# Kernel tuning notes

Hardware: AMD Instinct MI355X
Metric: run time of the kernel (lower is better)

## Reference

```python
import jax, jax.numpy as jnp
import numpy as np

N = 100000      # total nodes across batch of graphs
E = 1600000     # total edges (avg degree 16)
DIN = 16        # raw node feature dim
H = 128         # social_hidden_dim
HEADS = 4
DOUT = H // HEADS
LAYERS = 2
G = 64          # number of graphs in batch
FOUT = 256      # fusion_hidden_dim
NEG_SLOPE = 0.2


def layer_norm(x, g, b, eps=1e-5):
    mu = x.mean(-1, keepdims=True)
    var = ((x - mu) ** 2).mean(-1, keepdims=True)
    return (x - mu) / jnp.sqrt(var + eps) * g + b


def gat_conv(h, src, dst, W, a_src, a_dst, bias):
    # h: [N,H]; src/dst: [E+N] (self-loops included)
    hp = (h @ W).reshape(N, HEADS, DOUT)                    # [N,heads,dout]
    al_s = jnp.einsum('nhd,hd->nh', hp, a_src)              # [N,heads]
    al_d = jnp.einsum('nhd,hd->nh', hp, a_dst)
    logits = jax.nn.leaky_relu(al_s[src] + al_d[dst], NEG_SLOPE)  # [Etot,heads]
    m = jax.ops.segment_max(logits, dst, num_segments=N)    # segment softmax over dst
    e = jnp.exp(logits - m[dst])
    denom = jax.ops.segment_sum(e, dst, num_segments=N)
    alpha = e / (denom[dst] + 1e-16)                        # [Etot,heads]
    msg = hp[src] * alpha[:, :, None]                       # [Etot,heads,dout]
    out = jax.ops.segment_sum(msg, dst, num_segments=N)     # scatter-add
    return out.reshape(N, H) + bias


def setup_inputs():
    key = jax.random.key(0)
    ks = jax.random.split(key, 24)
    s = 0.05
    inp = {
        'x': jax.random.normal(ks[0], (N, DIN), jnp.float32),
        'edge_index': jax.random.randint(ks[1], (2, E), 0, N, jnp.int32),
        'node2graph': (jnp.arange(N, dtype=jnp.int32) * G // N).astype(jnp.int32),
        'Wp': jax.random.normal(ks[2], (DIN, H)) * s,
        'bp': jnp.zeros((H,)),
        'Wq1': jax.random.normal(ks[3], (2 * H, H)) * s,
        'bq1': jnp.zeros((H,)),
        'gq': jnp.ones((H,)), 'beq': jnp.zeros((H,)),
        'Wq2': jax.random.normal(ks[4], (H, FOUT)) * s,
        'bq2': jnp.zeros((FOUT,)),
    }
    for i in range(LAYERS):
        inp[f'Wg{i}'] = jax.random.normal(ks[5 + 4 * i], (H, H)) * s
        inp[f'as{i}'] = jax.random.normal(ks[6 + 4 * i], (HEADS, DOUT)) * s
        inp[f'ad{i}'] = jax.random.normal(ks[7 + 4 * i], (HEADS, DOUT)) * s
        inp[f'bg{i}'] = jnp.zeros((H,))
        inp[f'g{i}'] = jnp.ones((H,))
        inp[f'be{i}'] = jnp.zeros((H,))
    return inp


def reference(x, edge_index, node2graph, Wp, bp, Wq1, bq1, gq, beq, Wq2, bq2,
              Wg0, as0, ad0, bg0, g0, be0, Wg1, as1, ad1, bg1, g1, be1):
    loop = jnp.arange(N, dtype=edge_index.dtype)
    src = jnp.concatenate([edge_index[0], loop])  # add self-loops (PyG default)
    dst = jnp.concatenate([edge_index[1], loop])

    h = jax.nn.gelu(x @ Wp + bp, approximate=False)
    params = [(Wg0, as0, ad0, bg0, g0, be0), (Wg1, as1, ad1, bg1, g1, be1)]
    for (W, a_s, a_d, b, g, be) in params:
        h_new = gat_conv(h, src, dst, W, a_s, a_d, b)
        h = layer_norm(h_new + h, g, be)  # dims match -> residual

    counts = jax.ops.segment_sum(jnp.ones((N, 1), h.dtype), node2graph, num_segments=G)
    mean_pool = jax.ops.segment_sum(h, node2graph, num_segments=G) / jnp.maximum(counts, 1.0)
    max_pool = jax.ops.segment_max(h, node2graph, num_segments=G)
    emb = jnp.concatenate([mean_pool, max_pool], axis=-1)  # [G, 2H]

    p = layer_norm(emb @ Wq1 + bq1, gq, beq)
    p = jax.nn.gelu(p, approximate=False)
    return p @ Wq2 + bq2  # [G, FOUT]
```

## Files before the change

kernel.cpp:

```cpp
#include <hip/hip_runtime.h>

typedef unsigned short u16;
typedef unsigned char u8;
typedef unsigned int u32;
typedef unsigned long long u64;
typedef short short8 __attribute__((ext_vector_type(8)));
typedef float f32x4 __attribute__((ext_vector_type(4)));
typedef float f32x2 __attribute__((ext_vector_type(2)));

#define NN   100000
#define EE   1600000
#define ETOT (EE + NN)
#define NG   64
#define WSTR 136
#define SCANB 98
#define NB   98
#define BCAP 24576
#define OCAP 262144
#define EPB  4096

constexpr size_t AL256(size_t x) { return (x + 255) & ~(size_t)255; }
constexpr size_t OFF_FLAG   = 0;
constexpr size_t OFF_BSUM   = AL256(OFF_FLAG + 256);
constexpr size_t OFF_BCNT   = AL256(OFF_BSUM + 128 * 4);
constexpr size_t OFF_ROWPTR = AL256(OFF_BCNT + 128 * 4);
constexpr size_t OFF_DEG    = AL256(OFF_ROWPTR + (size_t)(NN + 1) * 4);
constexpr size_t OFF_COL    = AL256(OFF_DEG + (size_t)NN * 4);
constexpr size_t OFF_ALS    = AL256(OFF_COL + (size_t)ETOT * 4);
constexpr size_t OFF_ALD    = AL256(OFF_ALS + (size_t)NN * 4 * 4);
constexpr size_t OFF_GSUM   = AL256(OFF_ALD + (size_t)NN * 4 * 4);
constexpr size_t OFF_GKEY   = AL256(OFF_GSUM + (size_t)NG * 128 * 4);
constexpr size_t OFF_GCNT   = AL256(OFF_GKEY + (size_t)NG * 128 * 4);
constexpr size_t OFF_H      = AL256(OFF_GCNT + (size_t)NG * 4);
constexpr size_t OFF_HPB    = AL256(OFF_H + (size_t)NN * 128 * 2);
constexpr size_t OFF_EBUF   = AL256(OFF_HPB + (size_t)NN * 128 * 1);
constexpr size_t OFF_OBUF   = AL256(OFF_EBUF + (size_t)NB * BCAP * 8);
constexpr size_t WS_TOTAL   = AL256(OFF_OBUF + (size_t)OCAP * 8);

__device__ u64 g_ws[WS_TOTAL / 8];

__device__ __forceinline__ char* wsp() { return (char*)g_ws; }
#define WS_FLAG   ((int*)(wsp() + OFF_FLAG))
#define WS_BSUM   ((int*)(wsp() + OFF_BSUM))
#define WS_BCNT   ((int*)(wsp() + OFF_BCNT))
#define WS_ROWPTR ((int*)(wsp() + OFF_ROWPTR))
#define WS_DEG    ((int*)(wsp() + OFF_DEG))
#define WS_COL    ((int*)(wsp() + OFF_COL))
#define WS_ALS    ((float*)(wsp() + OFF_ALS))
#define WS_ALD    ((float*)(wsp() + OFF_ALD))
#define WS_GSUM   ((float*)(wsp() + OFF_GSUM))
#define WS_GKEY   ((u32*)(wsp() + OFF_GKEY))
#define WS_GCNT   ((int*)(wsp() + OFF_GCNT))
#define WS_H      ((u16*)(wsp() + OFF_H))
#define WS_HPB    ((u8*)(wsp() + OFF_HPB))
#define WS_EBUF   ((u64*)(wsp() + OFF_EBUF))
#define WS_OBUF   ((u64*)(wsp() + OFF_OBUF))

__device__ __forceinline__ float b2f(u16 u) { return __uint_as_float(((u32)u) << 16); }
__device__ __forceinline__ float b2f_lo(u32 u) { return __uint_as_float(u << 16); }
__device__ __forceinline__ float b2f_hi(u32 u) { return __uint_as_float(u & 0xffff0000u); }
__device__ __forceinline__ u16 f2bf(float f) {
    u32 u = __float_as_uint(f);
    return (u16)((u + 0x7fffu + ((u >> 16) & 1u)) >> 16);
}
__device__ __forceinline__ float ldf(const void* p, int i, int bf) {
    return bf ? b2f(((const u16*)p)[i]) : ((const float*)p)[i];
}
__device__ __forceinline__ int ldint(const int* p, long long i, int wide) {
    return wide ? p[i * 2] : p[(size_t)i];
}
__device__ __forceinline__ u32 fkey(float f) {
    u32 u = __float_as_uint(f);
    return (u >> 31) ? ~u : (u | 0x80000000u);
}
__device__ __forceinline__ float funkey(u32 k) {
    u32 u = (k & 0x80000000u) ? (k & 0x7fffffffu) : ~k;
    return __uint_as_float(u);
}

__global__ __launch_bounds__(256) void k_zero(const void* __restrict__ x,
                                              const int* __restrict__ ei) {
    if (blockIdx.x == 0 && threadIdx.x < 64) {
        int t = threadIdx.x;
        const u16* p = (const u16*)x;
        u16 u = p[t * 2];
        int e = (u >> 7) & 0xff;
        int ok = ((u & 0x7fffu) == 0) || (e >= 0x60 && e <= 0x9f);
        u64 m1 = __ballot(ok);
        int z = (ei[t * 2 + 1] == 0);
        u64 m2 = __ballot(z);
        if (t == 0) {
            WS_FLAG[0] = (__popcll(m1) >= 48) ? 1 : 0;
            WS_FLAG[1] = (__popcll(m2) >= 56) ? 1 : 0;
        }
    }
    if (blockIdx.x == 0 && threadIdx.x == 64) WS_FLAG[2] = 0;
    int i = blockIdx.x * 256 + threadIdx.x;
    if (i < NN) WS_DEG[i] = 0;
    if (i < NG * 128) { WS_GSUM[i] = 0.f; WS_GKEY[i] = 0u; }
    if (i < NG) WS_GCNT[i] = 0;
    if (i < NB) WS_BCNT[i] = 0;
}

__global__ __launch_bounds__(256) void k_bucket(const int* __restrict__ ei) {
    __shared__ int lcnt[NB], lbase[NB], lcur[NB];
    int t = threadIdx.x;
    int wide = WS_FLAG[1];
    for (int i = t; i < NB; i += 256) { lcnt[i] = 0; lcur[i] = 0; }
    __syncthreads();
    int e0 = blockIdx.x * EPB + t;
    int sA[16], dA[16];
#pragma unroll
    for (int j = 0; j < 16; j++) {
        int e = e0 + j * 256;
        int s = -1, d = 0;
        if (e < ETOT) {
            if (e < EE) {
                if (wide) { s = ((const int2*)ei)[e].x; d = ((const int2*)ei)[(size_t)EE + e].x; }
                else      { s = ei[e];                  d = ei[(size_t)EE + e]; }
            } else { s = e - EE; d = s; }
            if ((u32)s >= NN || (u32)d >= NN) s = -1;
        }
        sA[j] = s; dA[j] = d;
        if (s >= 0) atomicAdd(&lcnt[d >> 10], 1);
    }
    __syncthreads();
    for (int i = t; i < NB; i += 256)
        lbase[i] = atomicAdd(&WS_BCNT[i], lcnt[i]);
    __syncthreads();
    u64* ebuf = WS_EBUF;
#pragma unroll
    for (int j = 0; j < 16; j++) {
        int s = sA[j], d = dA[j];
        if (s < 0) continue;
        int b = d >> 10;
        int r = atomicAdd(&lcur[b], 1);
        int slot = lbase[b] + r;
        u64 pk = ((u64)(u32)d << 32) | (u32)s;
        if (slot < BCAP) {
            ebuf[(size_t)b * BCAP + slot] = pk;
        } else {
            int o = atomicAdd(&WS_FLAG[2], 1);
            if (o < OCAP) {
                WS_OBUF[o] = pk;
                atomicAdd(&WS_DEG[d], 1);
            }
        }
    }
}

__global__ __launch_bounds__(1024) void k_scan1() {
    __shared__ int sdat[1024];
    __shared__ int hist[1024];
    int b = blockIdx.x, t = threadIdx.x;
    hist[t] = 0;
    __syncthreads();
    int bc = WS_BCNT[b]; if (bc > BCAP) bc = BCAP;
    const u64* eb = WS_EBUF + (size_t)b * BCAP;
    for (int i = t; i < bc; i += 1024) {
        int d = (int)(eb[i] >> 32);
        atomicAdd(&hist[d & 1023], 1);
    }
    __syncthreads();
    int i = b * 1024 + t;
    int v = (i < NN) ? (WS_DEG[i] + hist[t]) : 0;
    sdat[t] = v;
    __syncthreads();
    for (int off = 1; off < 1024; off <<= 1) {
        int u = 0;
        if (t >= off) u = sdat[t - off];
        __syncthreads();
        if (t >= off) sdat[t] += u;
        __syncthreads();
    }
    if (i < NN) WS_ROWPTR[i] = sdat[t] - v;
    if (t == 1023) WS_BSUM[b] = sdat[1023];
}

__global__ __launch_bounds__(256) void k_place() {
    __shared__ int cur[1024];
    __shared__ int sb[128];
    int b = blockIdx.x, t = threadIdx.x;
    if (t < 128) sb[t] = (t < SCANB) ? WS_BSUM[t] : 0;
    __syncthreads();
    for (int off = 1; off < 128; off <<= 1) {
        int u = 0;
        if (t < 128 && t >= off) u = sb[t - off];
        __syncthreads();
        if (t < 128 && t >= off) sb[t] += u;
        __syncthreads();
    }
    int add = (b > 0) ? sb[b - 1] : 0;
    int n0 = b << 10;
    for (int i = t; i < 1024; i += 256) {
        int n = n0 + i;
        int r = 0;
        if (n < NN) {
            r = WS_ROWPTR[n] + add;
            WS_ROWPTR[n] = r;
        }
        cur[i] = r;
    }
    if (b == 0 && t == 0) WS_ROWPTR[NN] = sb[127];
    __syncthreads();
    int bc = WS_BCNT[b]; if (bc > BCAP) bc = BCAP;
    const u64* eb = WS_EBUF + (size_t)b * BCAP;
    for (int i = t; i < bc; i += 256) {
        u64 pk = eb[i];
        int d = (int)(pk >> 32), s = (int)(pk & 0xffffffffu);
        int pos = atomicAdd(&cur[d & 1023], 1);
        WS_COL[pos] = s;
    }
    int cnt = WS_FLAG[2]; if (cnt > OCAP) cnt = OCAP;
    for (int i = t; i < cnt; i += 256) {
        u64 pk = WS_OBUF[i];
        int d = (int)(pk >> 32);
        if ((d >> 10) == b) {
            int pos = atomicAdd(&cur[d & 1023], 1);
            WS_COL[pos] = (int)(pk & 0xffffffffu);
        }
    }
}

__global__ __launch_bounds__(128) void k_proj(const void* __restrict__ x,
                                              const void* __restrict__ Wp,
                                              const void* __restrict__ bp) {
    __shared__ float sW[16 * 128];
    int t = threadIdx.x;
    int bf = WS_FLAG[0];
    for (int i = t; i < 16 * 128; i += 128) sW[i] = ldf(Wp, i, bf);
    __syncthreads();
    float bj = ldf(bp, t, bf);
    for (int n = blockIdx.x; n < NN; n += gridDim.x) {
        float acc = bj;
#pragma unroll
        for (int k = 0; k < 16; k++)
            acc = fmaf(ldf(x, n * 16 + k, bf), sW[k * 128 + t], acc);
        float g = 0.5f * acc * (1.0f + erff(acc * 0.70710678118654752f));
        WS_H[(size_t)n * 128 + t] = f2bf(g);
    }
}

__global__ __launch_bounds__(256) void k_gemm(const void* __restrict__ Wg,
                                              const void* __restrict__ a_s,
                                              const void* __restrict__ a_d) {
    __shared__ __align__(16) u16 sWt[128 * WSTR];
    __shared__ __align__(16) u16 sH[16 * WSTR];
    int t = threadIdx.x;
    int bf = WS_FLAG[0];
    for (int idx = t; idx < 128 * 128; idx += 256) {
        int k = idx >> 7, n = idx & 127;
        sWt[n * WSTR + k] = bf ? ((const u16*)Wg)[idx] : f2bf(((const float*)Wg)[idx]);
    }
    __syncthreads();
    int wv = t >> 6, lane = t & 63;
    int n0 = wv * 32;
    int quad = lane >> 4, m16 = lane & 15;
    int ce = n0 + 2 * m16;
    float as0v = ldf(a_s, ce, bf),     as1v = ldf(a_s, ce + 1, bf);
    float ad0v = ldf(a_d, ce, bf),     ad1v = ldf(a_d, ce + 1, bf);
    short8 bfr[2][4];
#pragma unroll
    for (int nt = 0; nt < 2; nt++) {
        int n = ce + nt;
#pragma unroll
        for (int ks = 0; ks < 4; ks++)
            bfr[nt][ks] = *(const short8*)&sWt[n * WSTR + ks * 32 + quad * 8];
    }
    u8* hp = WS_HPB;
    const u32* h32 = (const u32*)WS_H;
    u32* sH32 = (u32*)sH;
    for (int m0 = blockIdx.x * 16; m0 < NN; m0 += gridDim.x * 16) {
        __syncthreads();
        for (int idx = t; idx < 16 * 64; idx += 256) {
            int r = idx >> 6, c2 = idx & 63;
            sH32[r * 68 + c2] = h32[(size_t)(m0 + r) * 64 + c2];
        }
        __syncthreads();
        f32x4 acc0 = {0.f, 0.f, 0.f, 0.f};
        f32x4 acc1 = {0.f, 0.f, 0.f, 0.f};
#pragma unroll
        for (int ks = 0; ks < 4; ks++) {
            short8 af = *(const short8*)&sH[m16 * WSTR + ks * 32 + quad * 8];
            acc0 = __builtin_amdgcn_mfma_f32_16x16x32_bf16(af, bfr[0][ks], acc0, 0, 0, 0);
            acc1 = __builtin_amdgcn_mfma_f32_16x16x32_bf16(af, bfr[1][ks], acc1, 0, 0, 0);
        }
#pragma unroll
        for (int r = 0; r < 4; r++) {
            size_t row = (size_t)(m0 + quad * 4 + r) * 128;
            u32 pk8 = (u32)__builtin_amdgcn_cvt_pk_fp8_f32(acc0[r], acc1[r], 0, false);
            *(u16*)&hp[row + ce] = (u16)(pk8 & 0xffffu);
            float ps = acc0[r] * as0v + acc1[r] * as1v;
            float pd = acc0[r] * ad0v + acc1[r] * ad1v;
#pragma unroll
            for (int m = 1; m <= 8; m <<= 1) {
                ps += __shfl_xor(ps, m);
                pd += __shfl_xor(pd, m);
            }
            if (m16 == 0) {
                int nrow = m0 + quad * 4 + r;
                WS_ALS[nrow * 4 + wv] = ps;
                WS_ALD[nrow * 4 + wv] = pd;
            }
        }
    }
}

__global__ __launch_bounds__(512) void k_gat(const void* __restrict__ bg,
                                             const void* __restrict__ gam,
                                             const void* __restrict__ bet) {
    int wid = threadIdx.x >> 6, lane = threadIdx.x & 63;
    int n = blockIdx.x * 8 + wid;
    if (n >= NN) return;
    int bf = WS_FLAG[0];
    const int* col = WS_COL;
    const float* als = WS_ALS;
    int k0 = WS_ROWPTR[n], deg = WS_ROWPTR[n + 1] - k0;
    int hd = lane >> 4, eo = lane & 15;
    float aldh = WS_ALD[n * 4 + hd];
    const u16* hp16 = (const u16*)WS_HPB;
    u32* h32 = (u32*)WS_H;
    u32 hv = h32[(size_t)n * 64 + lane];
    int base48 = lane & 48;

    int i0 = eo, i1 = eo + 16;
    int e0 = k0 + (i0 < deg ? i0 : 0);
    int e1 = k0 + (i1 < deg ? i1 : 0);
    int sc0 = col[e0];
    int sc1 = col[e1];
    float v0 = als[sc0 * 4 + hd] + aldh;
    float v1 = als[sc1 * 4 + hd] + aldh;
    v0 = v0 > 0.f ? v0 : 0.2f * v0;
    v1 = v1 > 0.f ? v1 : 0.2f * v1;
    float w0 = (i0 < deg) ? __expf(v0) : 0.f;
    float w1 = (i1 < deg) ? __expf(v1) : 0.f;
    float se = w0 + w1;
    float a0 = 0.f, a1 = 0.f;

#pragma unroll
    for (int j = 0; j < 16; j++) {
        float wj = __shfl(w0, base48 + j);
        int   sj = __builtin_amdgcn_readlane(sc0, j);
        u16 pv = hp16[(size_t)sj * 64 + lane];
        f32x2 mv = __builtin_amdgcn_cvt_pk_f32_fp8((int)pv, false);
        a0 = fmaf(wj, mv.x, a0);
        a1 = fmaf(wj, mv.y, a1);
    }
    if (deg > 16) {
#pragma unroll
        for (int j = 0; j < 16; j++) {
            float wj = __shfl(w1, base48 + j);
            int   sj = __builtin_amdgcn_readlane(sc1, j);
            u16 pv = hp16[(size_t)sj * 64 + lane];
            f32x2 mv = __builtin_amdgcn_cvt_pk_f32_fp8((int)pv, false);
            a0 = fmaf(wj, mv.x, a0);
            a1 = fmaf(wj, mv.y, a1);
        }
    }

    if (__builtin_expect(deg > 32, 0)) {
        for (int c = 32; c < deg; c += 16) {
            int i = c + eo;
            float w = 0.f; int scol = 0;
            if (i < deg) {
                scol = col[k0 + i];
                float v = als[scol * 4 + hd] + aldh;
                v = v > 0.f ? v : 0.2f * v;
                w = __expf(v);
            }
            se += w;
            int rem = deg - c; if (rem > 16) rem = 16;
            for (int j = 0; j < rem; j++) {
                float wj = __shfl(w, base48 + j);
                int sj = __shfl(scol, base48 + j);
                u16 pv = hp16[(size_t)sj * 64 + lane];
                f32x2 mv = __builtin_amdgcn_cvt_pk_f32_fp8((int)pv, false);
                a0 = fmaf(wj, mv.x, a0);
                a1 = fmaf(wj, mv.y, a1);
            }
        }
    }

    se += __shfl_xor(se, 1);
    se += __shfl_xor(se, 2);
    se += __shfl_xor(se, 4);
    se += __shfl_xor(se, 8);
    float inv = 1.f / (se + 1e-16f);
    int d0 = lane * 2, d1 = d0 + 1;
    float r0 = a0 * inv + ldf(bg, d0, bf) + b2f_lo(hv);
    float r1 = a1 * inv + ldf(bg, d1, bf) + b2f_hi(hv);
    float s1 = r0 + r1;
#pragma unroll
    for (int m = 1; m <= 32; m <<= 1) s1 += __shfl_xor(s1, m);
    float mu = s1 * (1.f / 128.f);
    float e0f = r0 - mu, e1f = r1 - mu;
    float s2 = e0f * e0f + e1f * e1f;
#pragma unroll
    for (int m = 1; m <= 32; m <<= 1) s2 += __shfl_xor(s2, m);
    float rstd = rsqrtf(s2 * (1.f / 128.f) + 1e-5f);
    float y0 = e0f * rstd * ldf(gam, d0, bf) + ldf(bet, d0, bf);
    float y1 = e1f * rstd * ldf(gam, d1, bf) + ldf(bet, d1, bf);
    h32[(size_t)n * 64 + lane] = (u32)f2bf(y0) | ((u32)f2bf(y1) << 16);
}

__global__ __launch_bounds__(128) void k_pool(const int* __restrict__ n2g) {
    int j = threadIdx.x;
    int wide = WS_FLAG[1];
    int n0 = blockIdx.x * 128;
    int n1 = n0 + 128; if (n1 > NN) n1 = NN;
    float runs = 0.f, runm = -3.4e38f;
    int rung = -1, runc = 0;
    for (int n = n0; n < n1; n++) {
        int g = ldint(n2g, n, wide);
        if (g != rung) {
            if (rung >= 0 && (u32)rung < NG) {
                atomicAdd(&WS_GSUM[rung * 128 + j], runs);
                atomicMax(&WS_GKEY[rung * 128 + j], fkey(runm));
                if (j == 0) atomicAdd(&WS_GCNT[rung], runc);
            }
            rung = g; runs = 0.f; runm = -3.4e38f; runc = 0;
        }
        float v = b2f(WS_H[(size_t)n * 128 + j]);
        runs += v;
        runm = fmaxf(runm, v);
        runc++;
    }
    if (rung >= 0 && (u32)rung < NG) {
        atomicAdd(&WS_GSUM[rung * 128 + j], runs);
        atomicMax(&WS_GKEY[rung * 128 + j], fkey(runm));
        if (j == 0) atomicAdd(&WS_GCNT[rung], runc);
    }
}

__global__ __launch_bounds__(256) void k_head(const void* __restrict__ Wq1,
                                              const void* __restrict__ bq1,
                                              const void* __restrict__ gq,
                                              const void* __restrict__ beq,
                                              const void* __restrict__ Wq2,
                                              const void* __restrict__ bq2,
                                              float* __restrict__ out) {
    __shared__ float sem[256];
    __shared__ float sp[128];
    __shared__ float red[4];
    int g = blockIdx.x, t = threadIdx.x;
    int bf = WS_FLAG[0];
    float cnt = fmaxf((float)WS_GCNT[g], 1.f);
    if (t < 128) sem[t] = WS_GSUM[g * 128 + t] / cnt;
    else         sem[t] = funkey(WS_GKEY[g * 128 + (t - 128)]);
    __syncthreads();
    float a = 0.f;
    if (t < 128) {
        a = ldf(bq1, t, bf);
        for (int k = 0; k < 256; k++) a = fmaf(sem[k], ldf(Wq1, k * 128 + t, bf), a);
    }
    int lane = t & 63, wv = t >> 6;
    float s1 = (t < 128) ? a : 0.f;
#pragma unroll
    for (int m = 1; m <= 32; m <<= 1) s1 += __shfl_xor(s1, m);
    if (lane == 0) red[wv] = s1;
    __syncthreads();
    float mu = (red[0] + red[1]) * (1.f / 128.f);
    float d = (t < 128) ? (a - mu) : 0.f;
    float s2 = d * d;
#pragma unroll
    for (int m = 1; m <= 32; m <<= 1) s2 += __shfl_xor(s2, m);
    __syncthreads();
    if (lane == 0) red[wv] = s2;
    __syncthreads();
    float var = (red[0] + red[1]) * (1.f / 128.f);
    if (t < 128) {
        float p = d * rsqrtf(var + 1e-5f) * ldf(gq, t, bf) + ldf(beq, t, bf);
        sp[t] = 0.5f * p * (1.0f + erff(p * 0.70710678118654752f));
    }
    __syncthreads();
    float o = ldf(bq2, t, bf);
    for (int k = 0; k < 128; k++)
        o = fmaf(sp[k], ldf(Wq2, k * 256 + t, bf), o);
    out[g * 256 + t] = o;
}

extern "C" void kernel_launch(void* const* d_in, const int* in_sizes, int n_in,
                              void* d_out, int out_size, void* d_ws, size_t ws_size,
                              hipStream_t stream) {
    const void* x   = d_in[0];
    const int* ei   = (const int*)d_in[1];
    const int* n2g  = (const int*)d_in[2];
    const void* Wp  = d_in[3];
    const void* bp  = d_in[4];
    const void* Wq1 = d_in[5];
    const void* bq1 = d_in[6];
    const void* gq  = d_in[7];
    const void* beq = d_in[8];
    const void* Wq2 = d_in[9];
    const void* bq2 = d_in[10];
    const void* Wg0 = d_in[11];
    const void* as0 = d_in[12];
    const void* ad0 = d_in[13];
    const void* bg0 = d_in[14];
    const void* g0  = d_in[15];
    const void* be0 = d_in[16];
    const void* Wg1 = d_in[17];
    const void* as1 = d_in[18];
    const void* ad1 = d_in[19];
    const void* bg1 = d_in[20];
    const void* g1  = d_in[21];
    const void* be1 = d_in[22];
    (void)d_ws; (void)ws_size; (void)in_sizes; (void)n_in; (void)out_size;

    k_zero<<<(NN + 255) / 256, 256, 0, stream>>>(x, ei);

    k_bucket<<<(ETOT + EPB - 1) / EPB, 256, 0, stream>>>(ei);
    k_scan1<<<SCANB, 1024, 0, stream>>>();
    k_place<<<NB, 256, 0, stream>>>();

    k_proj<<<2048, 128, 0, stream>>>(x, Wp, bp);

    k_gemm<<<1024, 256, 0, stream>>>(Wg0, as0, ad0);
    k_gat<<<(NN + 7) / 8, 512, 0, stream>>>(bg0, g0, be0);
    k_gemm<<<1024, 256, 0, stream>>>(Wg1, as1, ad1);
    k_gat<<<(NN + 7) / 8, 512, 0, stream>>>(bg1, g1, be1);

    k_pool<<<(NN + 127) / 128, 128, 0, stream>>>(n2g);
    k_head<<<NG, 256, 0, stream>>>(Wq1, bq1, gq, beq, Wq2, bq2, (float*)d_out);
}
```

Measured before the change: 543.2 us.

## Pack bucketed edges into 32 bits, use wave-shuffle scans, load GEMM A directly

Bucket entries now pack the local destination (10 bits) and the source (17 bits) into one 32-bit word instead of 64 bits, halving edge-buffer traffic in bucket, scan and place. The block-wide LDS Hillis-Steele scans in k_scan1 and k_place become wave-level shuffle scans with fewer barriers. k_gemm drops its LDS staging of H rows and barriers, reading MFMA A fragments straight from global memory, and its grid doubles. The direct loads may be less coalesced, and the packing relies on node ids fitting in 17 bits.

```diff
diff --git a/kernel.cpp b/kernel.cpp
--- a/kernel.cpp
+++ b/kernel.cpp
@@ -34,7 +34,7 @@
 constexpr size_t OFF_H      = AL256(OFF_GCNT + (size_t)NG * 4);
 constexpr size_t OFF_HPB    = AL256(OFF_H + (size_t)NN * 128 * 2);
 constexpr size_t OFF_EBUF   = AL256(OFF_HPB + (size_t)NN * 128 * 1);
-constexpr size_t OFF_OBUF   = AL256(OFF_EBUF + (size_t)NB * BCAP * 8);
+constexpr size_t OFF_OBUF   = AL256(OFF_EBUF + (size_t)NB * BCAP * 4);
 constexpr size_t WS_TOTAL   = AL256(OFF_OBUF + (size_t)OCAP * 8);
 
 __device__ u64 g_ws[WS_TOTAL / 8];
@@ -53,7 +53,7 @@
 #define WS_GCNT   ((int*)(wsp() + OFF_GCNT))
 #define WS_H      ((u16*)(wsp() + OFF_H))
 #define WS_HPB    ((u8*)(wsp() + OFF_HPB))
-#define WS_EBUF   ((u64*)(wsp() + OFF_EBUF))
+#define WS_EBUF   ((u32*)(wsp() + OFF_EBUF))
 #define WS_OBUF   ((u64*)(wsp() + OFF_OBUF))
 
 __device__ __forceinline__ float b2f(u16 u) { return __uint_as_float(((u32)u) << 16); }
@@ -128,7 +128,7 @@
     for (int i = t; i < NB; i += 256)
         lbase[i] = atomicAdd(&WS_BCNT[i], lcnt[i]);
     __syncthreads();
-    u64* ebuf = WS_EBUF;
+    u32* ebuf = WS_EBUF;
 #pragma unroll
     for (int j = 0; j < 16; j++) {
         int s = sA[j], d = dA[j];
@@ -136,13 +136,12 @@
         int b = d >> 10;
         int r = atomicAdd(&lcur[b], 1);
         int slot = lbase[b] + r;
-        u64 pk = ((u64)(u32)d << 32) | (u32)s;
         if (slot < BCAP) {
-            ebuf[(size_t)b * BCAP + slot] = pk;
+            ebuf[(size_t)b * BCAP + slot] = ((u32)(d & 1023) << 17) | (u32)s;
         } else {
             int o = atomicAdd(&WS_FLAG[2], 1);
             if (o < OCAP) {
-                WS_OBUF[o] = pk;
+                WS_OBUF[o] = ((u64)(u32)d << 32) | (u32)s;
                 atomicAdd(&WS_DEG[d], 1);
             }
         }
@@ -150,46 +149,61 @@
 }
 
 __global__ __launch_bounds__(1024) void k_scan1() {
-    __shared__ int sdat[1024];
     __shared__ int hist[1024];
+    __shared__ int wsum[16];
     int b = blockIdx.x, t = threadIdx.x;
     hist[t] = 0;
     __syncthreads();
     int bc = WS_BCNT[b]; if (bc > BCAP) bc = BCAP;
-    const u64* eb = WS_EBUF + (size_t)b * BCAP;
-    for (int i = t; i < bc; i += 1024) {
-        int d = (int)(eb[i] >> 32);
-        atomicAdd(&hist[d & 1023], 1);
-    }
+    const u32* eb = WS_EBUF + (size_t)b * BCAP;
+    for (int i = t; i < bc; i += 1024)
+        atomicAdd(&hist[eb[i] >> 17], 1);
     __syncthreads();
     int i = b * 1024 + t;
     int v = (i < NN) ? (WS_DEG[i] + hist[t]) : 0;
-    sdat[t] = v;
-    __syncthreads();
-    for (int off = 1; off < 1024; off <<= 1) {
-        int u = 0;
-        if (t >= off) u = sdat[t - off];
-        __syncthreads();
-        if (t >= off) sdat[t] += u;
-        __syncthreads();
-    }
-    if (i < NN) WS_ROWPTR[i] = sdat[t] - v;
-    if (t == 1023) WS_BSUM[b] = sdat[1023];
+    int lane = t & 63, wv = t >> 6;
+    int x = v;
+#pragma unroll
+    for (int off = 1; off < 64; off <<= 1) {
+        int y = __shfl_up(x, off);
+        if (lane >= off) x += y;
+    }
+    if (lane == 63) wsum[wv] = x;
+    __syncthreads();
+    if (wv == 0 && lane < 16) {
+        int y = wsum[lane];
+#pragma unroll
+        for (int off = 1; off < 16; off <<= 1) {
+            int z = __shfl_up(y, off);
+            if (lane >= off) y += z;
+        }
+        wsum[lane] = y;
+    }
+    __syncthreads();
+    int incl = x + (wv > 0 ? wsum[wv - 1] : 0);
+    if (i < NN) WS_ROWPTR[i] = incl - v;
+    if (t == 1023) WS_BSUM[b] = incl;
 }
 
 __global__ __launch_bounds__(256) void k_place() {
     __shared__ int cur[1024];
     __shared__ int sb[128];
+    __shared__ int w0tot;
     int b = blockIdx.x, t = threadIdx.x;
-    if (t < 128) sb[t] = (t < SCANB) ? WS_BSUM[t] : 0;
-    __syncthreads();
-    for (int off = 1; off < 128; off <<= 1) {
-        int u = 0;
-        if (t < 128 && t >= off) u = sb[t - off];
-        __syncthreads();
-        if (t < 128 && t >= off) sb[t] += u;
-        __syncthreads();
-    }
+    int lane = t & 63;
+    if (t < 128) {
+        int x = (t < SCANB) ? WS_BSUM[t] : 0;
+#pragma unroll
+        for (int off = 1; off < 64; off <<= 1) {
+            int y = __shfl_up(x, off);
+            if (lane >= off) x += y;
+        }
+        if (t == 63) w0tot = x;
+        sb[t] = x;
+    }
+    __syncthreads();
+    if (t >= 64 && t < 128) sb[t] += w0tot;
+    __syncthreads();
     int add = (b > 0) ? sb[b - 1] : 0;
     int n0 = b << 10;
     for (int i = t; i < 1024; i += 256) {
@@ -204,11 +218,11 @@
     if (b == 0 && t == 0) WS_ROWPTR[NN] = sb[127];
     __syncthreads();
     int bc = WS_BCNT[b]; if (bc > BCAP) bc = BCAP;
-    const u64* eb = WS_EBUF + (size_t)b * BCAP;
+    const u32* eb = WS_EBUF + (size_t)b * BCAP;
     for (int i = t; i < bc; i += 256) {
-        u64 pk = eb[i];
-        int d = (int)(pk >> 32), s = (int)(pk & 0xffffffffu);
-        int pos = atomicAdd(&cur[d & 1023], 1);
+        u32 pk = eb[i];
+        int dl = pk >> 17, s = (int)(pk & 0x1ffffu);
+        int pos = atomicAdd(&cur[dl], 1);
         WS_COL[pos] = s;
     }
     int cnt = WS_FLAG[2]; if (cnt > OCAP) cnt = OCAP;
@@ -245,7 +259,6 @@
                                               const void* __restrict__ a_s,
                                               const void* __restrict__ a_d) {
     __shared__ __align__(16) u16 sWt[128 * WSTR];
-    __shared__ __align__(16) u16 sH[16 * WSTR];
     int t = threadIdx.x;
     int bf = WS_FLAG[0];
     for (int idx = t; idx < 128 * 128; idx += 256) {
@@ -268,20 +281,14 @@
             bfr[nt][ks] = *(const short8*)&sWt[n * WSTR + ks * 32 + quad * 8];
     }
     u8* hp = WS_HPB;
-    const u32* h32 = (const u32*)WS_H;
-    u32* sH32 = (u32*)sH;
+    const u16* hsrc = WS_H;
     for (int m0 = blockIdx.x * 16; m0 < NN; m0 += gridDim.x * 16) {
-        __syncthreads();
-        for (int idx = t; idx < 16 * 64; idx += 256) {
-            int r = idx >> 6, c2 = idx & 63;
-            sH32[r * 68 + c2] = h32[(size_t)(m0 + r) * 64 + c2];
-        }
-        __syncthreads();
+        const u16* arow = &hsrc[(size_t)(m0 + m16) * 128];
         f32x4 acc0 = {0.f, 0.f, 0.f, 0.f};
         f32x4 acc1 = {0.f, 0.f, 0.f, 0.f};
 #pragma unroll
         for (int ks = 0; ks < 4; ks++) {
-            short8 af = *(const short8*)&sH[m16 * WSTR + ks * 32 + quad * 8];
+            short8 af = *(const short8*)&arow[ks * 32 + quad * 8];
             acc0 = __builtin_amdgcn_mfma_f32_16x16x32_bf16(af, bfr[0][ks], acc0, 0, 0, 0);
             acc1 = __builtin_amdgcn_mfma_f32_16x16x32_bf16(af, bfr[1][ks], acc1, 0, 0, 0);
         }
@@ -515,9 +522,9 @@
 
     k_proj<<<2048, 128, 0, stream>>>(x, Wp, bp);
 
-    k_gemm<<<1024, 256, 0, stream>>>(Wg0, as0, ad0);
+    k_gemm<<<2048, 256, 0, stream>>>(Wg0, as0, ad0);
     k_gat<<<(NN + 7) / 8, 512, 0, stream>>>(bg0, g0, be0);
-    k_gemm<<<1024, 256, 0, stream>>>(Wg1, as1, ad1);
+    k_gemm<<<2048, 256, 0, stream>>>(Wg1, as1, ad1);
     k_gat<<<(NN + 7) / 8, 512, 0, stream>>>(bg1, g1, be1);
 
     k_pool<<<(NN + 127) / 128, 128, 0, stream>>>(n2g);
```

New measurement: 551.4 us. About the same (+1.5%).
